# Kernel optimization log

Hardware: AMD Instinct MI355X
Metric: run time of the kernel (lower is better)

The kernel has to match this reference:

```python
import jax, jax.numpy as jnp
import numpy as np

N, D, E = 16384, 2048, 64   # tokens, d_model, num_experts
K = 9                        # self.k = min(k+1, num_experts) with k=8
EPS = 0.01
SIGMA = 1.0 / E              # Normal(0, 1/num_experts) stddev


def setup_inputs() -> dict:
    key = jax.random.key(0)
    ks = jax.random.split(key, 6)
    x = jax.random.normal(ks[0], (N, D), jnp.float32)
    Wr = jax.random.normal(ks[1], (D, E), jnp.float32) * 0.02
    br = jnp.zeros((E,), jnp.float32)
    Wn = jax.random.normal(ks[2], (D, E), jnp.float32) * 0.02
    bn = jnp.zeros((E,), jnp.float32)
    noise_eps = jax.random.normal(ks[3], (N, E), jnp.float32)
    # torch: (-empty.exponential_()).log() -> log of Exp(1) samples
    gumbel_noise = jnp.log(jax.random.exponential(ks[4], (N, E), jnp.float32))
    return {"x": x, "Wr": Wr, "br": br, "Wn": Wn, "bn": bn,
            "noise_eps": noise_eps, "gumbel_noise": gumbel_noise}


def reference(x, Wr, br, Wn, bn, noise_eps, gumbel_noise):
    raw_logits = x @ Wr + br                              # [N, E]
    noise_stddev = jax.nn.softplus(x @ Wn + bn) + EPS     # [N, E]
    noisy_logits = raw_logits + noise_eps * noise_stddev  # [N, E]

    top_vals, top_idx = jax.lax.top_k(noisy_logits, K)    # [N, K] sorted desc
    # scatter ones at top-k indices (indices unique per row)
    hard_mask = jax.nn.one_hot(top_idx, E, dtype=noisy_logits.dtype).sum(axis=1)  # [N, E]

    # gumbel-softmax straight-through relaxation
    mask_soft = jax.nn.softmax(noisy_logits + gumbel_noise, axis=-1)
    expert_mask = hard_mask - jax.lax.stop_gradient(mask_soft) + mask_soft

    route_prob = jax.nn.softmax(noisy_logits, axis=-1)    # [N, E]
    importance = jax.nn.softmax(raw_logits, axis=-1).sum(axis=0)  # [E]

    # load: P(raw + noise > threshold), Normal(0, 1/E) CDF per original
    threshold = top_vals[:, K - 1]                        # [N]
    z = (threshold[:, None] - raw_logits) / noise_stddev  # [N, E]
    cdf = 0.5 * (1.0 + jax.scipy.special.erf(z / (SIGMA * jnp.sqrt(jnp.float32(2.0)))))
    load = (1.0 - cdf).sum(axis=0)                        # [E]

    return (expert_mask, route_prob, importance, load)
```

## Files before the change

### kernel.cpp

```cpp
#include <hip/hip_runtime.h>
#include <hip/hip_bf16.h>
#include <math.h>

#define N_TOK 16384
#define DIM   2048
#define NE    64
#define TOPK  9

#define ROWS     32
#define DC       64
#define NCHUNK   (DIM / DC)
#define NTHREADS 256

typedef short  short8  __attribute__((ext_vector_type(8)));
typedef float  float4_ __attribute__((ext_vector_type(4)));
typedef unsigned short ushort_t;

__device__ __forceinline__ void async16(const void* g, void* l) {
    __builtin_amdgcn_global_load_lds(
        (const __attribute__((address_space(1))) void*)g,
        (__attribute__((address_space(3))) void*)l, 16, 0, 0);
}

__device__ __forceinline__ unsigned pk2(float a, float b) {
    float2 f; f.x = a; f.y = b;
    __hip_bfloat162 h = __float22bfloat162_rn(f);
    unsigned u;
    __builtin_memcpy(&u, &h, 4);
    return u;
}

__device__ __forceinline__ void cvt8(const float4_ va, const float4_ vb,
                                     short8* h, short8* l) {
    union { short8 s; unsigned u[4]; } H, L;
    const float f[8] = {va[0], va[1], va[2], va[3], vb[0], vb[1], vb[2], vb[3]};
#pragma unroll
    for (int i = 0; i < 4; ++i) {
        const float a = f[2 * i], b = f[2 * i + 1];
        const unsigned p = pk2(a, b);
        H.u[i] = p;
        const float ha = __uint_as_float(p << 16);
        const float hb = __uint_as_float(p & 0xffff0000u);
        L.u[i] = pk2(a - ha, b - hb);
    }
    *h = H.s; *l = L.s;
}

__device__ __forceinline__ float wave_max64(float v) {
#pragma unroll
    for (int off = 32; off > 0; off >>= 1)
        v = fmaxf(v, __shfl_xor(v, off, 64));
    return v;
}
__device__ __forceinline__ float wave_sum64(float v) {
#pragma unroll
    for (int off = 32; off > 0; off >>= 1)
        v += __shfl_xor(v, off, 64);
    return v;
}

__global__ __launch_bounds__(256)
void prep_w(const float* __restrict__ Wr, const float* __restrict__ Wn,
            ushort_t* __restrict__ wsW)
{
    const int gid = blockIdx.x * 256 + threadIdx.x;
    const int l   = gid & 63;
    const int ct  = (gid >> 6) & 7;
    const int kcg = gid >> 9;
    const int n   = ct * 16 + (l & 15);
    const int k0  = kcg * 32 + (l >> 4) * 8;
    const float* src = (n < NE) ? (Wr + n) : (Wn + (n - NE));
    union { short8 s; ushort_t us[8]; } H, L;
#pragma unroll
    for (int j = 0; j < 8; ++j) {
        const float v = src[(size_t)(k0 + j) * NE];
        const unsigned uv = __float_as_uint(v);
        const unsigned hb = (uv + 0x7fffu + ((uv >> 16) & 1u)) & 0xffff0000u;
        const float lo = v - __uint_as_float(hb);
        const unsigned ul = __float_as_uint(lo);
        H.us[j] = (ushort_t)(hb >> 16);
        L.us[j] = (ushort_t)((ul + 0x7fffu + ((ul >> 16) & 1u)) >> 16);
    }
    const size_t s0 = (size_t)(kcg * 8 + ct) * 2;
    *(short8*)(wsW + s0 * 512 + l * 8)         = H.s;
    *(short8*)(wsW + (s0 + 1) * 512 + l * 8)   = L.s;
}

__global__ __launch_bounds__(NTHREADS, 3)
void moe_main(const float* __restrict__ x,
              const float* __restrict__ br,
              const float* __restrict__ bn,
              const float* __restrict__ noise_eps,
              const float* __restrict__ gumbel,
              const ushort_t* __restrict__ wsW,
              float* __restrict__ out)
{
    __shared__ __align__(16) float smem[4352];

    const int t    = threadIdx.x;
    const int lane = t & 63;
    const int w    = t >> 6;
    const int c4   = lane & 15;
    const int q    = lane >> 4;
    const int row0 = blockIdx.x * ROWS;

    const float* gxp[2];
    int lxo[2];
#pragma unroll
    for (int ii = 0; ii < 2; ++ii) {
        const int i  = 2 * w + ii;
        const int r  = 4 * i + q;
        const int gk = c4 ^ (r & 15);
        gxp[ii] = x + (size_t)(row0 + r) * DIM + gk * 4;
        lxo[ii] = i * 256;
    }

    int aoff[2][2];
#pragma unroll
    for (int kc = 0; kc < 2; ++kc) {
        const int g0 = kc * 8 + q * 2;
        aoff[kc][0] = c4 * 64 + ((g0 ^ c4) * 4);
        aoff[kc][1] = c4 * 64 + (((g0 + 1) ^ c4) * 4);
    }

    float4_ acc[2][2];
#pragma unroll
    for (int rt = 0; rt < 2; ++rt)
#pragma unroll
        for (int cc = 0; cc < 2; ++cc)
            acc[rt][cc] = (float4_)(0.f);

    const char* wsB = (const char*)wsW;

#pragma unroll
    for (int ii = 0; ii < 2; ++ii) { async16(gxp[ii], &smem[lxo[ii]]); gxp[ii] += DC; }

    for (int ch = 0; ch < NCHUNK; ++ch) {
        __syncthreads();
        const int b = ch & 1;
        short8 bh[2][2], bl[2][2];
#pragma unroll
        for (int kc = 0; kc < 2; ++kc)
#pragma unroll
            for (int cc = 0; cc < 2; ++cc) {
                const size_t off = (size_t)(((ch * 2 + kc) * 8) + 2 * w + cc) * 2048 + lane * 16;
                bh[kc][cc] = *(const short8*)(wsB + off);
                bl[kc][cc] = *(const short8*)(wsB + off + 1024);
            }
        if (ch + 1 < NCHUNK) {
#pragma unroll
            for (int ii = 0; ii < 2; ++ii) {
                async16(gxp[ii], &smem[(b ^ 1) * 2048 + lxo[ii]]);
                gxp[ii] += DC;
            }
        }
        const float* xb = &smem[b * 2048];
#pragma unroll
        for (int kc = 0; kc < 2; ++kc)
#pragma unroll
            for (int rt = 0; rt < 2; ++rt) {
                const float4_ va = *(const float4_*)(xb + rt * 1024 + aoff[kc][0]);
                const float4_ vb = *(const float4_*)(xb + rt * 1024 + aoff[kc][1]);
                short8 ah, al;
                cvt8(va, vb, &ah, &al);
#pragma unroll
                for (int cc = 0; cc < 2; ++cc) {
                    acc[rt][cc] = __builtin_amdgcn_mfma_f32_16x16x32_bf16(ah, bh[kc][cc], acc[rt][cc], 0, 0, 0);
                    acc[rt][cc] = __builtin_amdgcn_mfma_f32_16x16x32_bf16(al, bh[kc][cc], acc[rt][cc], 0, 0, 0);
                    acc[rt][cc] = __builtin_amdgcn_mfma_f32_16x16x32_bf16(ah, bl[kc][cc], acc[rt][cc], 0, 0, 0);
                }
            }
    }

    __syncthreads();
    float* rawS = &smem[0];
    float* noiS = &smem[2080];
#pragma unroll
    for (int rt = 0; rt < 2; ++rt)
#pragma unroll
        for (int cc = 0; cc < 2; ++cc) {
            const int colg = (2 * w + cc) * 16 + c4;
            float* basep = (colg < NE) ? rawS : noiS;
            const int col = colg & 63;
#pragma unroll
            for (int v = 0; v < 4; ++v) {
                const int row = rt * 16 + q * 4 + v;
                basep[row * 65 + col] = acc[rt][cc][v];
            }
        }
    __syncthreads();

    const float br_l = br[lane];
    const float bn_l = bn[lane];
    float imp_acc = 0.f, load_acc = 0.f;
    float* out_em   = out;
    float* out_rp   = out + (size_t)N_TOK * NE;
    float* out_imp  = out + (size_t)2 * N_TOK * NE;
    float* out_load = out_imp + NE;

#pragma unroll 1
    for (int r = 0; r < 8; ++r) {
        const int lrow = w * 8 + r;
        const int row  = row0 + lrow;
        const float raw = rawS[lrow * 65 + lane] + br_l;
        const float nl  = noiS[lrow * 65 + lane] + bn_l;
        const float sd = fmaxf(nl, 0.f) + log1pf(expf(-fabsf(nl))) + 0.01f;
        const float epsv = noise_eps[(size_t)row * NE + lane];
        const float gum  = gumbel  [(size_t)row * NE + lane];
        const float noisy = fmaf(epsv, sd, raw);

        float cur = noisy;
        float thr = 0.f, m0 = 0.f;
#pragma unroll 1
        for (int k = 0; k < TOPK; ++k) {
            const float m = wave_max64(cur);
            if (k == 0) m0 = m;
            thr = m;
            const unsigned long long bm = __ballot(cur == m);
            const int first = __ffsll(bm) - 1;
            if (lane == first) cur = -INFINITY;
        }
        const float hard = (noisy >= thr) ? 1.f : 0.f;

        const float g  = noisy + gum;
        const float eg = expf(g - wave_max64(g));
        const float ms = eg / wave_sum64(eg);
        const float em = (hard - ms) + ms;

        const float en = expf(noisy - m0);
        const float rp = en / wave_sum64(en);

        const float er = expf(raw - wave_max64(raw));
        imp_acc += er / wave_sum64(er);

        const float z = (thr - raw) / sd;
        load_acc += 0.5f * erfcf(z * 45.254833995939045f);

        out_em[(size_t)row * NE + lane] = em;
        out_rp[(size_t)row * NE + lane] = rp;
    }

    __syncthreads();
    smem[w * 64 + lane]       = imp_acc;
    smem[256 + w * 64 + lane] = load_acc;
    __syncthreads();
    if (w == 0) {
        const float s1 = smem[lane] + smem[64 + lane] + smem[128 + lane] + smem[192 + lane];
        const float s2 = smem[256 + lane] + smem[320 + lane] + smem[384 + lane] + smem[448 + lane];
        atomicAdd(&out_imp[lane], s1);
        atomicAdd(&out_load[lane], s2);
    }
}

extern "C" void kernel_launch(void* const* d_in, const int* in_sizes, int n_in,
                              void* d_out, int out_size, void* d_ws, size_t ws_size,
                              hipStream_t stream)
{
    const float* x         = (const float*)d_in[0];
    const float* Wr        = (const float*)d_in[1];
    const float* br        = (const float*)d_in[2];
    const float* Wn        = (const float*)d_in[3];
    const float* bn        = (const float*)d_in[4];
    const float* noise_eps = (const float*)d_in[5];
    const float* gumbel    = (const float*)d_in[6];
    float* out = (float*)d_out;
    ushort_t* wsW = (ushort_t*)d_ws;

    (void)hipMemsetAsync((char*)d_out + (size_t)2 * N_TOK * NE * sizeof(float), 0,
                         2 * NE * sizeof(float), stream);
    prep_w<<<128, 256, 0, stream>>>(Wr, Wn, wsW);
    moe_main<<<N_TOK / ROWS, NTHREADS, 0, stream>>>(
        x, br, bn, noise_eps, gumbel, wsW, out);
}
```

Measured before the change: 268.5 us.

## Use 64-row 512-thread blocks, direct global A loads, and radix top-k select

Doubles rows per block to 64 and threads to 512, splitting eight waves into row and column groups. x is now read straight from global memory into registers instead of through async LDS double buffering, which removes the per-chunk barriers. The 9-step argmax top-k becomes a 32-bit radix select built on ballot and popcount. Noise loads are hoisted out of the row loop, and the wave max and sum reductions are batched. The softmax for route_prob now subtracts the top-k threshold instead of the row maximum, which is mathematically equivalent but could overflow if the maximum is far above the threshold. Uncoalesced direct x loads may also cost bandwidth.

Measured after the change: 278.4 us. 3.7% more time.

```diff
diff --git a/kernel.cpp b/kernel.cpp
--- a/kernel.cpp
+++ b/kernel.cpp
@@ -7,20 +7,14 @@
 #define NE    64
 #define TOPK  9
 
-#define ROWS     32
+#define ROWS     64
 #define DC       64
 #define NCHUNK   (DIM / DC)
-#define NTHREADS 256
+#define NTHREADS 512
 
 typedef short  short8  __attribute__((ext_vector_type(8)));
 typedef float  float4_ __attribute__((ext_vector_type(4)));
 typedef unsigned short ushort_t;
-
-__device__ __forceinline__ void async16(const void* g, void* l) {
-    __builtin_amdgcn_global_load_lds(
-        (const __attribute__((address_space(1))) void*)g,
-        (__attribute__((address_space(3))) void*)l, 16, 0, 0);
-}
 
 __device__ __forceinline__ unsigned pk2(float a, float b) {
     float2 f; f.x = a; f.y = b;
@@ -46,17 +40,26 @@
     *h = H.s; *l = L.s;
 }
 
-__device__ __forceinline__ float wave_max64(float v) {
-#pragma unroll
-    for (int off = 32; off > 0; off >>= 1)
-        v = fmaxf(v, __shfl_xor(v, off, 64));
-    return v;
-}
-__device__ __forceinline__ float wave_sum64(float v) {
-#pragma unroll
-    for (int off = 32; off > 0; off >>= 1)
-        v += __shfl_xor(v, off, 64);
-    return v;
+__device__ __forceinline__ void wave_max64_2(float& a, float& b) {
+#pragma unroll
+    for (int off = 32; off > 0; off >>= 1) {
+        const float ax = __shfl_xor(a, off, 64);
+        const float bx = __shfl_xor(b, off, 64);
+        a = fmaxf(a, ax);
+        b = fmaxf(b, bx);
+    }
+}
+
+__device__ __forceinline__ void wave_sum64_3(float& a, float& b, float& c) {
+#pragma unroll
+    for (int off = 32; off > 0; off >>= 1) {
+        const float ax = __shfl_xor(a, off, 64);
+        const float bx = __shfl_xor(b, off, 64);
+        const float cx = __shfl_xor(c, off, 64);
+        a += ax;
+        b += bx;
+        c += cx;
+    }
 }
 
 __global__ __launch_bounds__(256)
@@ -86,7 +89,7 @@
     *(short8*)(wsW + (s0 + 1) * 512 + l * 8)   = L.s;
 }
 
-__global__ __launch_bounds__(NTHREADS, 3)
+__global__ __launch_bounds__(NTHREADS, 2)
 void moe_main(const float* __restrict__ x,
               const float* __restrict__ br,
               const float* __restrict__ bn,
@@ -95,33 +98,21 @@
               const ushort_t* __restrict__ wsW,
               float* __restrict__ out)
 {
-    __shared__ __align__(16) float smem[4352];
+    __shared__ __align__(16) float smem[8320];
 
     const int t    = threadIdx.x;
     const int lane = t & 63;
     const int w    = t >> 6;
     const int c4   = lane & 15;
     const int q    = lane >> 4;
+    const int rg   = w >> 2;
+    const int cg   = w & 3;
     const int row0 = blockIdx.x * ROWS;
 
-    const float* gxp[2];
-    int lxo[2];
-#pragma unroll
-    for (int ii = 0; ii < 2; ++ii) {
-        const int i  = 2 * w + ii;
-        const int r  = 4 * i + q;
-        const int gk = c4 ^ (r & 15);
-        gxp[ii] = x + (size_t)(row0 + r) * DIM + gk * 4;
-        lxo[ii] = i * 256;
-    }
-
-    int aoff[2][2];
-#pragma unroll
-    for (int kc = 0; kc < 2; ++kc) {
-        const int g0 = kc * 8 + q * 2;
-        aoff[kc][0] = c4 * 64 + ((g0 ^ c4) * 4);
-        aoff[kc][1] = c4 * 64 + (((g0 + 1) ^ c4) * 4);
-    }
+    const float* pA[2];
+#pragma unroll
+    for (int rt = 0; rt < 2; ++rt)
+        pA[rt] = x + (size_t)(row0 + (2 * rg + rt) * 16 + c4) * DIM + q * 8;
 
     float4_ acc[2][2];
 #pragma unroll
@@ -132,35 +123,25 @@
 
     const char* wsB = (const char*)wsW;
 
-#pragma unroll
-    for (int ii = 0; ii < 2; ++ii) { async16(gxp[ii], &smem[lxo[ii]]); gxp[ii] += DC; }
-
+#pragma unroll 2
     for (int ch = 0; ch < NCHUNK; ++ch) {
-        __syncthreads();
-        const int b = ch & 1;
         short8 bh[2][2], bl[2][2];
 #pragma unroll
         for (int kc = 0; kc < 2; ++kc)
 #pragma unroll
             for (int cc = 0; cc < 2; ++cc) {
-                const size_t off = (size_t)(((ch * 2 + kc) * 8) + 2 * w + cc) * 2048 + lane * 16;
+                const int ct = 2 * cg + cc;
+                const size_t off = (size_t)(((ch * 2 + kc) * 8) + ct) * 2048
+                                 + (size_t)lane * 16;
                 bh[kc][cc] = *(const short8*)(wsB + off);
                 bl[kc][cc] = *(const short8*)(wsB + off + 1024);
             }
-        if (ch + 1 < NCHUNK) {
-#pragma unroll
-            for (int ii = 0; ii < 2; ++ii) {
-                async16(gxp[ii], &smem[(b ^ 1) * 2048 + lxo[ii]]);
-                gxp[ii] += DC;
-            }
-        }
-        const float* xb = &smem[b * 2048];
 #pragma unroll
         for (int kc = 0; kc < 2; ++kc)
 #pragma unroll
             for (int rt = 0; rt < 2; ++rt) {
-                const float4_ va = *(const float4_*)(xb + rt * 1024 + aoff[kc][0]);
-                const float4_ vb = *(const float4_*)(xb + rt * 1024 + aoff[kc][1]);
+                const float4_ va = *(const float4_*)(pA[rt] + ch * DC + kc * 32);
+                const float4_ vb = *(const float4_*)(pA[rt] + ch * DC + kc * 32 + 4);
                 short8 ah, al;
                 cvt8(va, vb, &ah, &al);
 #pragma unroll
@@ -172,19 +153,18 @@
             }
     }
 
-    __syncthreads();
     float* rawS = &smem[0];
-    float* noiS = &smem[2080];
+    float* noiS = &smem[4160];
 #pragma unroll
     for (int rt = 0; rt < 2; ++rt)
 #pragma unroll
         for (int cc = 0; cc < 2; ++cc) {
-            const int colg = (2 * w + cc) * 16 + c4;
+            const int colg = (2 * cg + cc) * 16 + c4;
             float* basep = (colg < NE) ? rawS : noiS;
             const int col = colg & 63;
 #pragma unroll
             for (int v = 0; v < 4; ++v) {
-                const int row = rt * 16 + q * 4 + v;
+                const int row = (2 * rg + rt) * 16 + q * 4 + v;
                 basep[row * 65 + col] = acc[rt][cc][v];
             }
         }
@@ -192,6 +172,15 @@
 
     const float br_l = br[lane];
     const float bn_l = bn[lane];
+
+    float epsv[8], gumv[8];
+#pragma unroll
+    for (int r = 0; r < 8; ++r) {
+        const int row = row0 + w * 8 + r;
+        epsv[r] = noise_eps[(size_t)row * NE + lane];
+        gumv[r] = gumbel  [(size_t)row * NE + lane];
+    }
+
     float imp_acc = 0.f, load_acc = 0.f;
     float* out_em   = out;
     float* out_rp   = out + (size_t)N_TOK * NE;
@@ -205,33 +194,34 @@
         const float raw = rawS[lrow * 65 + lane] + br_l;
         const float nl  = noiS[lrow * 65 + lane] + bn_l;
         const float sd = fmaxf(nl, 0.f) + log1pf(expf(-fabsf(nl))) + 0.01f;
-        const float epsv = noise_eps[(size_t)row * NE + lane];
-        const float gum  = gumbel  [(size_t)row * NE + lane];
-        const float noisy = fmaf(epsv, sd, raw);
-
-        float cur = noisy;
-        float thr = 0.f, m0 = 0.f;
-#pragma unroll 1
-        for (int k = 0; k < TOPK; ++k) {
-            const float m = wave_max64(cur);
-            if (k == 0) m0 = m;
-            thr = m;
-            const unsigned long long bm = __ballot(cur == m);
-            const int first = __ffsll(bm) - 1;
-            if (lane == first) cur = -INFINITY;
+        const float noisy = fmaf(epsv[r], sd, raw);
+
+        const unsigned uk  = __float_as_uint(noisy);
+        const unsigned key = uk ^ ((uk & 0x80000000u) ? 0xFFFFFFFFu : 0x80000000u);
+        unsigned res = 0;
+#pragma unroll
+        for (int bit = 31; bit >= 0; --bit) {
+            const unsigned cand = res | (1u << bit);
+            const int cnt = __popcll(__ballot(key >= cand));
+            if (cnt >= TOPK) res = cand;
         }
-        const float hard = (noisy >= thr) ? 1.f : 0.f;
-
-        const float g  = noisy + gum;
-        const float eg = expf(g - wave_max64(g));
-        const float ms = eg / wave_sum64(eg);
+        const float thr  = __uint_as_float(res ^ ((res & 0x80000000u) ? 0x80000000u : 0xFFFFFFFFu));
+        const float hard = (key >= res) ? 1.f : 0.f;
+
+        const float g = noisy + gumv[r];
+        float mg = g, mr = raw;
+        wave_max64_2(mg, mr);
+
+        const float eg = expf(g - mg);
+        const float en = expf(noisy - thr);
+        const float er = expf(raw - mr);
+        float sg = eg, sn = en, sr = er;
+        wave_sum64_3(sg, sn, sr);
+
+        const float ms = eg / sg;
         const float em = (hard - ms) + ms;
-
-        const float en = expf(noisy - m0);
-        const float rp = en / wave_sum64(en);
-
-        const float er = expf(raw - wave_max64(raw));
-        imp_acc += er / wave_sum64(er);
+        const float rp = en / sn;
+        imp_acc += er / sr;
 
         const float z = (thr - raw) / sd;
         load_acc += 0.5f * erfcf(z * 45.254833995939045f);
@@ -242,11 +232,15 @@
 
     __syncthreads();
     smem[w * 64 + lane]       = imp_acc;
-    smem[256 + w * 64 + lane] = load_acc;
+    smem[512 + w * 64 + lane] = load_acc;
     __syncthreads();
     if (w == 0) {
-        const float s1 = smem[lane] + smem[64 + lane] + smem[128 + lane] + smem[192 + lane];
-        const float s2 = smem[256 + lane] + smem[320 + lane] + smem[384 + lane] + smem[448 + lane];
+        float s1 = 0.f, s2 = 0.f;
+#pragma unroll
+        for (int i = 0; i < 8; ++i) {
+            s1 += smem[i * 64 + lane];
+            s2 += smem[512 + i * 64 + lane];
+        }
         atomicAdd(&out_imp[lane], s1);
         atomicAdd(&out_load[lane], s2);
     }
```
